# Optimization experiments

Measured on AMD Instinct MI355X. Metric: run time of the kernel, lower is better.

The kernel has to match this reference:

```python
import jax, jax.numpy as jnp
from jax import lax
import numpy as np

# LeNet-5 C3 sparse connectivity table (which S2 maps feed each C3 map)
IDX3 = np.array([[0,1,2],[1,2,3],[2,3,4],[3,4,5],[0,4,5],[0,1,5]])            # maps 0-5 (3 inputs)
IDX4 = np.array([[0,1,2,3],[1,2,3,4],[2,3,4,5],[0,3,4,5],[0,1,4,5],
                 [0,1,2,5],[0,1,3,4],[1,2,4,5],[0,2,3,5]])                    # maps 6-14 (4 inputs)


def _conv(x, w):
    return lax.conv_general_dilated(x, w, (1, 1), 'VALID',
                                    dimension_numbers=('NCHW', 'OIHW', 'NCHW'))


def _avgpool2(x):
    s = lax.reduce_window(x, 0.0, lax.add, (1, 1, 2, 2), (1, 1, 2, 2), 'VALID')
    return s * 0.25


def setup_inputs() -> dict:
    key = jax.random.key(0)
    ks = jax.random.split(key, 12)
    f = lambda k, shp: (jax.random.normal(k, shp, dtype=jnp.float32) * 0.1)
    return {
        'x':     jax.random.normal(ks[0], (8192, 1, 32, 32), dtype=jnp.float32),
        'c1_w':  f(ks[1], (6, 1, 5, 5)),   'c1_b': f(ks[2], (6,)),
        'c3_w3': f(ks[3], (6, 3, 5, 5)),   'c3_b3': f(ks[4], (6,)),
        'c3_w4': f(ks[5], (9, 4, 5, 5)),   'c3_b4': f(ks[6], (9,)),
        'c3_w6': f(ks[7], (1, 6, 5, 5)),   'c3_b6': f(ks[8], (1,)),
        'c5_w':  f(ks[9], (120, 16, 5, 5)), 'c5_b': f(ks[10], (120,)),
        'l1_w':  f(ks[11], (84, 120)), 'l1_b': jnp.zeros((84,), jnp.float32),
        'l2_w':  f(jax.random.fold_in(key, 99), (10, 84)), 'l2_b': jnp.zeros((10,), jnp.float32),
    }


def reference(x, c1_w, c1_b, c3_w3, c3_b3, c3_w4, c3_b4, c3_w6, c3_b6,
              c5_w, c5_b, l1_w, l1_b, l2_w, l2_b):
    # C1 + tanh + S2: [B,1,32,32] -> [B,6,14,14]
    out = jnp.tanh(_conv(x, c1_w) + c1_b[None, :, None, None])
    out = _avgpool2(out)

    # C3: fuse the 16 sparse-connectivity convs into one [16,6,5,5] conv
    # by scattering the small per-map kernels into a zero-padded weight.
    W = jnp.zeros((16, 6, 5, 5), dtype=out.dtype)
    W = W.at[np.arange(6)[:, None], IDX3].set(c3_w3)
    W = W.at[np.arange(6, 15)[:, None], IDX4].set(c3_w4)
    W = W.at[15].set(c3_w6[0])
    b = jnp.concatenate([c3_b3, c3_b4, c3_b6])
    out = _conv(out, W) + b[None, :, None, None]          # [B,16,10,10]

    out = _avgpool2(jnp.tanh(out))                        # [B,16,5,5]
    out = _conv(out, c5_w) + c5_b[None, :, None, None]    # [B,120,1,1]
    out = jnp.tanh(out[:, :, 0, 0])                       # [B,120]
    out = jnp.tanh(out @ l1_w.T + l1_b)                   # [B,84]
    return out @ l2_w.T + l2_b                            # [B,10]
```

## Files before the change

### kernel.cpp

```cpp
#include <hip/hip_runtime.h>

typedef float f32x4 __attribute__((ext_vector_type(4)));
typedef _Float16 h16;
typedef h16 half8 __attribute__((ext_vector_type(8)));

__device__ __forceinline__ float fast_tanh(float x) {
    float e = __expf(2.0f * x);
    return fmaf(-2.0f, __builtin_amdgcn_rcpf(e + 1.0f), 1.0f);
}
__device__ __forceinline__ half8 cvt8(float4 u0, float4 u1) {
    return (half8){(h16)u0.x,(h16)u0.y,(h16)u0.z,(h16)u0.w,
                   (h16)u1.x,(h16)u1.y,(h16)u1.z,(h16)u1.w};
}

#define S2IMGH 1576

#define C1_IMG 8

__global__ __launch_bounds__(256) void k_c1(
    const float* __restrict__ x, const float* __restrict__ c1_w,
    const float* __restrict__ c1_b, h16* __restrict__ s2g, int B)
{
    __shared__ __align__(16) h16 s2l[C1_IMG * S2IMGH];
    __shared__ float c1w_s[152];
    __shared__ float c1b_s[8];

    const int tid  = threadIdx.x;
    const int img0 = blockIdx.x * C1_IMG;
    const int nimg = min(C1_IMG, B - img0);
    if (nimg <= 0) return;

    if (tid < 150) c1w_s[tid] = c1_w[tid];
    if (tid < 6)   c1b_s[tid] = c1_b[tid];
    {
        const half8 z = {(h16)0,(h16)0,(h16)0,(h16)0,(h16)0,(h16)0,(h16)0,(h16)0};
        half8* zp = (half8*)s2l;
        for (int i = tid; i < C1_IMG * 197; i += 256) zp[i] = z;
    }
    __syncthreads();

    const int lane = tid & 63, wv = tid >> 6;
    const int nloc = lane & 15, q4 = lane >> 4;

    half8 bf[3][5];
    float bias[3];
    #pragma unroll
    for (int t = 0; t < 3; ++t) {
        const int tile = 3 * wv + t;
        const int map  = tile >> 1;
        const int j    = ((tile & 1) << 4) + nloc;
        bias[t] = c1b_s[map];
        #pragma unroll
        for (int ks = 0; ks < 5; ++ks) {
            half8 f;
            #pragma unroll
            for (int jj = 0; jj < 8; ++jj) {
                const int d = q4 * 8 + jj - j;
                f[jj] = (d >= 0 && d < 5) ? (h16)c1w_s[map * 25 + ks * 5 + d] : (h16)0;
            }
            bf[t][ks] = f;
        }
    }

    const int imgL = nloc >> 1, hf = nloc & 1;
    const int imgC = min(imgL, nimg - 1);
    const float* xg = x + (size_t)(img0 + imgC) * 1024 + hf * (14 * 32) + q4 * 8;
    half8 rf[5];
    #pragma unroll
    for (int r = 0; r < 5; ++r)
        rf[r] = cvt8(*(const float4*)(xg + r * 32), *(const float4*)(xg + r * 32 + 4));

    float t0[3][4];
    for (int cr = 0; cr < 14; ++cr) {
        f32x4 acc[3];
        #pragma unroll
        for (int t = 0; t < 3; ++t) acc[t] = (f32x4){0.f, 0.f, 0.f, 0.f};
        #pragma unroll
        for (int ks = 0; ks < 5; ++ks) {
            #pragma unroll
            for (int t = 0; t < 3; ++t)
                acc[t] = __builtin_amdgcn_mfma_f32_16x16x32_f16(rf[ks], bf[t][ks], acc[t], 0, 0, 0);
        }
        if ((cr & 1) == 0) {
            #pragma unroll
            for (int t = 0; t < 3; ++t)
                #pragma unroll
                for (int r = 0; r < 4; ++r)
                    t0[t][r] = fast_tanh(acc[t][r] + bias[t]);
        } else {
            #pragma unroll
            for (int t = 0; t < 3; ++t) {
                const int tile = 3 * wv + t;
                const int jp   = (((tile & 1) << 4) + nloc) >> 1;
                const int map  = tile >> 1;
                #pragma unroll
                for (int r = 0; r < 4; ++r) {
                    float s = t0[t][r] + fast_tanh(acc[t][r] + bias[t]);
                    float o = 0.25f * (s + __shfl_xor(s, 1));
                    const int m = q4 * 4 + r;
                    const int img = m >> 1, mh = m & 1;
                    const int ip  = (cr >> 1) + 7 * mh;
                    if (!(lane & 1) && jp < 14)
                        s2l[img * S2IMGH + (ip * 14 + jp) * 8 + map] = (h16)o;
                }
            }
        }
        if (cr < 13) {
            rf[0] = rf[1]; rf[1] = rf[2]; rf[2] = rf[3]; rf[3] = rf[4];
            rf[4] = cvt8(*(const float4*)(xg + (cr + 5) * 32),
                         *(const float4*)(xg + (cr + 5) * 32 + 4));
        }
    }
    __syncthreads();

    for (int i = tid; i < C1_IMG * 197; i += 256) {
        const int img = i / 197, c = i % 197;
        if (img < nimg)
            *(half8*)(s2g + (size_t)(img0 + img) * S2IMGH + c * 8) =
                *(const half8*)(s2l + img * S2IMGH + c * 8);
    }
}

__device__ __constant__ int C3_INV[16][6] = {
    {0,1,2,-1,-1,-1},{-1,0,1,2,-1,-1},{-1,-1,0,1,2,-1},{-1,-1,-1,0,1,2},
    {0,-1,-1,-1,1,2},{0,1,-1,-1,-1,2},
    {0,1,2,3,-1,-1},{-1,0,1,2,3,-1},{-1,-1,0,1,2,3},{0,-1,-1,1,2,3},
    {0,1,-1,-1,2,3},{0,1,2,-1,-1,3},{0,1,-1,2,3,-1},{-1,0,1,-1,2,3},
    {0,-1,1,2,-1,3},
    {0,1,2,3,4,5}
};

__global__ __launch_bounds__(256) void k_c3(
    const h16* __restrict__ s2g,
    const float* __restrict__ c3_w3, const float* __restrict__ c3_b3,
    const float* __restrict__ c3_w4, const float* __restrict__ c3_b4,
    const float* __restrict__ c3_w6, const float* __restrict__ c3_b6,
    h16* __restrict__ s4g, int B)
{
    __shared__ __align__(16) h16 s2i[16 * S2IMGH];

    const int tid  = threadIdx.x;
    const int img0 = blockIdx.x * 16;
    const int nimg = min(16, B - img0);
    if (nimg <= 0) return;

    {
        const half8 z = {(h16)0,(h16)0,(h16)0,(h16)0,(h16)0,(h16)0,(h16)0,(h16)0};
        const int img = tid >> 4;
        for (int c = (tid & 15); c < 197; c += 16)
            *(half8*)(s2i + img * S2IMGH + c * 8) =
                (img < nimg) ? *(const half8*)(s2g + (size_t)(img0 + img) * S2IMGH + c * 8)
                             : z;
    }

    const int lane = tid & 63, wv = tid >> 6;
    const int nloc = lane & 15, q4 = lane >> 4;

    half8 bf[7];
    #pragma unroll
    for (int t = 0; t < 7; ++t) {
        half8 f;
        int dr, dc; bool valid = true;
        if (t <= 4)      { dr = q4; dc = t; }
        else if (t == 5) { dr = 4; dc = q4; }
        else             { dr = 4; dc = 4; valid = (q4 == 0); }
        #pragma unroll
        for (int j = 0; j < 8; ++j) {
            float val = 0.0f;
            if (valid && j < 6) {
                const int cc = C3_INV[nloc][j];
                if (cc >= 0) {
                    const int off = dr * 5 + dc;
                    if (nloc < 6)       val = c3_w3[(nloc * 3 + cc) * 25 + off];
                    else if (nloc < 15) val = c3_w4[((nloc - 6) * 4 + cc) * 25 + off];
                    else                val = c3_w6[cc * 25 + off];
                }
            }
            f[j] = (h16)val;
        }
        bf[t] = f;
    }
    const float bias = (nloc < 6) ? c3_b3[nloc]
                     : (nloc < 15) ? c3_b4[nloc - 6] : c3_b6[0];
    __syncthreads();

    {
        const int abase = nloc * S2IMGH;
        for (int q = wv; q < 25; q += 4) {
            const int pr = q / 5, pc = q % 5;
            f32x4 acc[2][2];
            #pragma unroll
            for (int a = 0; a < 2; ++a)
                #pragma unroll
                for (int b2 = 0; b2 < 2; ++b2)
                    acc[a][b2] = (f32x4){0.f, 0.f, 0.f, 0.f};
            #pragma unroll
            for (int a = 0; a < 2; ++a) {
                #pragma unroll
                for (int b2 = 0; b2 < 2; ++b2) {
                    const int r = 2 * pr + a, col = 2 * pc + b2;
                    #pragma unroll
                    for (int t = 0; t < 5; ++t) {
                        half8 A = *(const half8*)(s2i + abase + ((r + q4) * 14 + col + t) * 8);
                        acc[a][b2] = __builtin_amdgcn_mfma_f32_16x16x32_f16(A, bf[t], acc[a][b2], 0, 0, 0);
                    }
                    half8 A5 = *(const half8*)(s2i + abase + ((r + 4) * 14 + col + q4) * 8);
                    acc[a][b2] = __builtin_amdgcn_mfma_f32_16x16x32_f16(A5, bf[5], acc[a][b2], 0, 0, 0);
                    half8 A6 = *(const half8*)(s2i + abase + ((r + 4) * 14 + col + 4) * 8);
                    acc[a][b2] = __builtin_amdgcn_mfma_f32_16x16x32_f16(A6, bf[6], acc[a][b2], 0, 0, 0);
                }
            }
            const int pos = pr * 5 + pc;
            #pragma unroll
            for (int rr = 0; rr < 4; ++rr) {
                const int img = q4 * 4 + rr;
                if (img < nimg) {
                    float s = fast_tanh(acc[0][0][rr] + bias) + fast_tanh(acc[0][1][rr] + bias)
                            + fast_tanh(acc[1][0][rr] + bias) + fast_tanh(acc[1][1][rr] + bias);
                    s4g[(size_t)(img0 + img) * 400 + nloc * 25 + pos] = (h16)(0.25f * s);
                }
            }
        }
    }
}

#define KT_IMG   16
#define S4L_STR  424
#define C5O_STR  136
#define F6L_STR  104
#define KT_S4L   0
#define KT_C5OL  (KT_IMG * S4L_STR * 2)
#define KT_F6L   (KT_C5OL + KT_IMG * C5O_STR * 2)
#define KT_BIAS  (KT_F6L + KT_IMG * F6L_STR * 2)
#define KT_SMEM  (KT_BIAS + 240 * 4)

__global__ __launch_bounds__(256) void k_tail(
    const h16* __restrict__ s4g,
    const float* __restrict__ c5_w, const float* __restrict__ c5_b,
    const float* __restrict__ l1_w, const float* __restrict__ l1_b,
    const float* __restrict__ l2_w, const float* __restrict__ l2_b,
    float* __restrict__ out, int B)
{
    __shared__ __align__(16) char smem[KT_SMEM];
    h16*   s4l   = (h16*)(smem + KT_S4L);
    h16*   c5ol  = (h16*)(smem + KT_C5OL);
    h16*   f6l   = (h16*)(smem + KT_F6L);
    float* c5b_s = (float*)(smem + KT_BIAS);
    float* l1b_s = c5b_s + 128;
    float* l2b_s = l1b_s + 96;

    const int tid  = threadIdx.x;
    const int img0 = blockIdx.x * KT_IMG;
    const int nimg = min(KT_IMG, B - img0);
    if (nimg <= 0) return;

    if (tid < 128)      c5b_s[tid] = (tid < 120) ? c5_b[tid] : 0.f;
    else if (tid < 224) { int i = tid - 128; l1b_s[i] = (i < 84) ? l1_b[i] : 0.f; }
    else if (tid < 240) { int i = tid - 224; l2b_s[i] = (i < 10) ? l2_b[i] : 0.f; }

    {
        const half8 z = {(h16)0,(h16)0,(h16)0,(h16)0,(h16)0,(h16)0,(h16)0,(h16)0};
        for (int i = tid; i < KT_IMG * 53; i += 256) {
            int img = i / 53, cc = i % 53;
            half8 v = z;
            if (img < nimg && cc < 50)
                v = *(const half8*)(s4g + (size_t)(img0 + img) * 400 + cc * 8);
            *(half8*)(s4l + img * S4L_STR + cc * 8) = v;
        }
    }
    __syncthreads();

    const int lane = tid & 63, wv = tid >> 6;
    const int nloc = lane & 15, q4 = lane >> 4;
    const half8 z8 = {(h16)0,(h16)0,(h16)0,(h16)0,(h16)0,(h16)0,(h16)0,(h16)0};

    {
        const int nb = wv * 2;
        f32x4 acc[2];
        acc[0] = (f32x4){0.f,0.f,0.f,0.f};
        acc[1] = (f32x4){0.f,0.f,0.f,0.f};
        for (int ks = 0; ks < 13; ++ks) {
            const int ka = ks * 32 + q4 * 8;
            half8 A = *(const half8*)(s4l + nloc * S4L_STR + ka);
            #pragma unroll
            for (int t = 0; t < 2; ++t) {
                const int n = (nb + t) * 16 + nloc;
                half8 Bf = z8;
                if (n < 120 && ka < 400) {
                    float4 u0 = *(const float4*)(c5_w + n * 400 + ka);
                    float4 u1 = *(const float4*)(c5_w + n * 400 + ka + 4);
                    Bf = cvt8(u0, u1);
                }
                acc[t] = __builtin_amdgcn_mfma_f32_16x16x32_f16(A, Bf, acc[t], 0, 0, 0);
            }
        }
        #pragma unroll
        for (int t = 0; t < 2; ++t) {
            const int o = (nb + t) * 16 + nloc;
            const float bo = c5b_s[o];
            #pragma unroll
            for (int r = 0; r < 4; ++r) {
                const int img = q4 * 4 + r;
                c5ol[img * C5O_STR + o] = (h16)fast_tanh(acc[t][r] + bo);
            }
        }
    }
    __syncthreads();

    if (wv < 3) {
        const int nb = wv * 2;
        f32x4 acc[2];
        acc[0] = (f32x4){0.f,0.f,0.f,0.f};
        acc[1] = (f32x4){0.f,0.f,0.f,0.f};
        for (int ks = 0; ks < 4; ++ks) {
            const int ka = ks * 32 + q4 * 8;
            half8 A = *(const half8*)(c5ol + nloc * C5O_STR + ka);
            #pragma unroll
            for (int t = 0; t < 2; ++t) {
                const int n = (nb + t) * 16 + nloc;
                half8 Bf = z8;
                if (n < 84 && ka < 120) {
                    float4 u0 = *(const float4*)(l1_w + n * 120 + ka);
                    float4 u1 = *(const float4*)(l1_w + n * 120 + ka + 4);
                    Bf = cvt8(u0, u1);
                }
                acc[t] = __builtin_amdgcn_mfma_f32_16x16x32_f16(A, Bf, acc[t], 0, 0, 0);
            }
        }
        #pragma unroll
        for (int t = 0; t < 2; ++t) {
            const int o = (nb + t) * 16 + nloc;
            const float bo = l1b_s[o];
            #pragma unroll
            for (int r = 0; r < 4; ++r) {
                const int img = q4 * 4 + r;
                f6l[img * F6L_STR + o] = (h16)fast_tanh(acc[t][r] + bo);
            }
        }
    }
    __syncthreads();

    if (wv == 0) {
        f32x4 acc = (f32x4){0.f,0.f,0.f,0.f};
        #pragma unroll
        for (int ks = 0; ks < 3; ++ks) {
            const int ka = ks * 32 + q4 * 8;
            half8 A = *(const half8*)(f6l + nloc * F6L_STR + ka);
            half8 Bf = z8;
            #pragma unroll
            for (int i = 0; i < 8; ++i) {
                const int k = ka + i;
                if (nloc < 10 && k < 84) Bf[i] = (h16)l2_w[nloc * 84 + k];
            }
            acc = __builtin_amdgcn_mfma_f32_16x16x32_f16(A, Bf, acc, 0, 0, 0);
        }
        if (nloc < 10) {
            #pragma unroll
            for (int r = 0; r < 4; ++r) {
                const int img = q4 * 4 + r;
                if (img < nimg)
                    out[(size_t)(img0 + img) * 10 + nloc] = acc[r] + l2b_s[nloc];
            }
        }
    }
}

extern "C" void kernel_launch(void* const* d_in, const int* in_sizes, int n_in,
                              void* d_out, int out_size, void* d_ws, size_t ws_size,
                              hipStream_t stream) {
    const float* x     = (const float*)d_in[0];
    const float* c1_w  = (const float*)d_in[1];
    const float* c1_b  = (const float*)d_in[2];
    const float* c3_w3 = (const float*)d_in[3];
    const float* c3_b3 = (const float*)d_in[4];
    const float* c3_w4 = (const float*)d_in[5];
    const float* c3_b4 = (const float*)d_in[6];
    const float* c3_w6 = (const float*)d_in[7];
    const float* c3_b6 = (const float*)d_in[8];
    const float* c5_w  = (const float*)d_in[9];
    const float* c5_b  = (const float*)d_in[10];
    const float* l1_w  = (const float*)d_in[11];
    const float* l1_b  = (const float*)d_in[12];
    const float* l2_w  = (const float*)d_in[13];
    const float* l2_b  = (const float*)d_in[14];
    float* out = (float*)d_out;

    const int B = in_sizes[0] / 1024;

    h16* s2g = (h16*)d_ws;
    h16* s4g = (h16*)((char*)d_ws + (size_t)B * S2IMGH * 2);

    k_c1<<<(B + C1_IMG - 1) / C1_IMG, 256, 0, stream>>>(x, c1_w, c1_b, s2g, B);
    k_c3<<<(B + 15) / 16, 256, 0, stream>>>(s2g, c3_w3, c3_b3, c3_w4, c3_b4,
                                            c3_w6, c3_b6, s4g, B);
    k_tail<<<(B + KT_IMG - 1) / KT_IMG, 256, 0, stream>>>(s4g, c5_w, c5_b,
                                                          l1_w, l1_b, l2_w, l2_b, out, B);
}
```

Measured before the change: 191.2 us.

## Split C1 and C3 blocks into two spatial halves to double grid size

```diff
diff --git a/kernel.cpp b/kernel.cpp
--- a/kernel.cpp
+++ b/kernel.cpp
@@ -17,69 +17,29 @@
 
 #define C1_IMG 8
 
-__global__ __launch_bounds__(256) void k_c1(
-    const float* __restrict__ x, const float* __restrict__ c1_w,
-    const float* __restrict__ c1_b, h16* __restrict__ s2g, int B)
+template<int BASE, int NITER>
+__device__ __forceinline__ void c1_phase(
+    const float* __restrict__ xg, const half8 (&bf)[3][5], const float (&bias)[3],
+    h16* __restrict__ s2l, int lane, int wv, int nloc, int q4)
 {
-    __shared__ __align__(16) h16 s2l[C1_IMG * S2IMGH];
-    __shared__ float c1w_s[152];
-    __shared__ float c1b_s[8];
-
-    const int tid  = threadIdx.x;
-    const int img0 = blockIdx.x * C1_IMG;
-    const int nimg = min(C1_IMG, B - img0);
-    if (nimg <= 0) return;
-
-    if (tid < 150) c1w_s[tid] = c1_w[tid];
-    if (tid < 6)   c1b_s[tid] = c1_b[tid];
-    {
-        const half8 z = {(h16)0,(h16)0,(h16)0,(h16)0,(h16)0,(h16)0,(h16)0,(h16)0};
-        half8* zp = (half8*)s2l;
-        for (int i = tid; i < C1_IMG * 197; i += 256) zp[i] = z;
-    }
-    __syncthreads();
-
-    const int lane = tid & 63, wv = tid >> 6;
-    const int nloc = lane & 15, q4 = lane >> 4;
-
-    half8 bf[3][5];
-    float bias[3];
+    half8 rw[NITER + 4];
     #pragma unroll
-    for (int t = 0; t < 3; ++t) {
-        const int tile = 3 * wv + t;
-        const int map  = tile >> 1;
-        const int j    = ((tile & 1) << 4) + nloc;
-        bias[t] = c1b_s[map];
+    for (int r = 0; r < NITER + 4; ++r)
+        rw[r] = cvt8(*(const float4*)(xg + (BASE + r) * 32),
+                     *(const float4*)(xg + (BASE + r) * 32 + 4));
+
+    float t0[3][4];
+    #pragma unroll
+    for (int cc = 0; cc < NITER; ++cc) {
+        const int cr = BASE + cc;
+        f32x4 acc[3];
+        #pragma unroll
+        for (int t = 0; t < 3; ++t) acc[t] = (f32x4){0.f, 0.f, 0.f, 0.f};
         #pragma unroll
         for (int ks = 0; ks < 5; ++ks) {
-            half8 f;
-            #pragma unroll
-            for (int jj = 0; jj < 8; ++jj) {
-                const int d = q4 * 8 + jj - j;
-                f[jj] = (d >= 0 && d < 5) ? (h16)c1w_s[map * 25 + ks * 5 + d] : (h16)0;
-            }
-            bf[t][ks] = f;
-        }
-    }
-
-    const int imgL = nloc >> 1, hf = nloc & 1;
-    const int imgC = min(imgL, nimg - 1);
-    const float* xg = x + (size_t)(img0 + imgC) * 1024 + hf * (14 * 32) + q4 * 8;
-    half8 rf[5];
-    #pragma unroll
-    for (int r = 0; r < 5; ++r)
-        rf[r] = cvt8(*(const float4*)(xg + r * 32), *(const float4*)(xg + r * 32 + 4));
-
-    float t0[3][4];
-    for (int cr = 0; cr < 14; ++cr) {
-        f32x4 acc[3];
-        #pragma unroll
-        for (int t = 0; t < 3; ++t) acc[t] = (f32x4){0.f, 0.f, 0.f, 0.f};
-        #pragma unroll
-        for (int ks = 0; ks < 5; ++ks) {
             #pragma unroll
             for (int t = 0; t < 3; ++t)
-                acc[t] = __builtin_amdgcn_mfma_f32_16x16x32_f16(rf[ks], bf[t][ks], acc[t], 0, 0, 0);
+                acc[t] = __builtin_amdgcn_mfma_f32_16x16x32_f16(rw[cc + ks], bf[t][ks], acc[t], 0, 0, 0);
         }
         if ((cr & 1) == 0) {
             #pragma unroll
@@ -105,19 +65,71 @@
                 }
             }
         }
-        if (cr < 13) {
-            rf[0] = rf[1]; rf[1] = rf[2]; rf[2] = rf[3]; rf[3] = rf[4];
-            rf[4] = cvt8(*(const float4*)(xg + (cr + 5) * 32),
-                         *(const float4*)(xg + (cr + 5) * 32 + 4));
-        }
-    }
-    __syncthreads();
-
-    for (int i = tid; i < C1_IMG * 197; i += 256) {
-        const int img = i / 197, c = i % 197;
+    }
+}
+
+__global__ __launch_bounds__(256) void k_c1(
+    const float* __restrict__ x, const float* __restrict__ c1_w,
+    const float* __restrict__ c1_b, h16* __restrict__ s2g, int B)
+{
+    __shared__ __align__(16) h16 s2l[C1_IMG * S2IMGH];
+    __shared__ float c1w_s[152];
+    __shared__ float c1b_s[8];
+
+    const int tid  = threadIdx.x;
+    const int ph   = blockIdx.x & 1;
+    const int img0 = (blockIdx.x >> 1) * C1_IMG;
+    const int nimg = min(C1_IMG, B - img0);
+    if (nimg <= 0) return;
+
+    if (tid < 150) c1w_s[tid] = c1_w[tid];
+    if (tid < 6)   c1b_s[tid] = c1_b[tid];
+    {
+        const half8 z = {(h16)0,(h16)0,(h16)0,(h16)0,(h16)0,(h16)0,(h16)0,(h16)0};
+        half8* zp = (half8*)s2l;
+        for (int i = tid; i < C1_IMG * 197; i += 256) zp[i] = z;
+    }
+    __syncthreads();
+
+    const int lane = tid & 63, wv = tid >> 6;
+    const int nloc = lane & 15, q4 = lane >> 4;
+
+    half8 bf[3][5];
+    float bias[3];
+    #pragma unroll
+    for (int t = 0; t < 3; ++t) {
+        const int tile = 3 * wv + t;
+        const int map  = tile >> 1;
+        const int j    = ((tile & 1) << 4) + nloc;
+        bias[t] = c1b_s[map];
+        #pragma unroll
+        for (int ks = 0; ks < 5; ++ks) {
+            half8 f;
+            #pragma unroll
+            for (int jj = 0; jj < 8; ++jj) {
+                const int d = q4 * 8 + jj - j;
+                f[jj] = (d >= 0 && d < 5) ? (h16)c1w_s[map * 25 + ks * 5 + d] : (h16)0;
+            }
+            bf[t][ks] = f;
+        }
+    }
+
+    const int imgL = nloc >> 1, hf = nloc & 1;
+    const int imgC = min(imgL, nimg - 1);
+    const float* xg = x + (size_t)(img0 + imgC) * 1024 + hf * (14 * 32) + q4 * 8;
+
+    if (ph == 0) c1_phase<0, 8>(xg, bf, bias, s2l, lane, wv, nloc, q4);
+    else         c1_phase<8, 6>(xg, bf, bias, s2l, lane, wv, nloc, q4);
+    __syncthreads();
+
+    const int nch = ph ? 84 : 112;
+    for (int i = tid; i < C1_IMG * nch; i += 256) {
+        const int img = i / nch, ii = i % nch;
+        const int pos = ph ? (ii < 42 ? 56 + ii : 112 + ii)
+                           : (ii < 56 ? ii : 42 + ii);
         if (img < nimg)
-            *(half8*)(s2g + (size_t)(img0 + img) * S2IMGH + c * 8) =
-                *(const half8*)(s2l + img * S2IMGH + c * 8);
+            *(half8*)(s2g + (size_t)(img0 + img) * S2IMGH + pos * 8) =
+                *(const half8*)(s2l + img * S2IMGH + pos * 8);
     }
 }
 
@@ -140,7 +152,8 @@
     __shared__ __align__(16) h16 s2i[16 * S2IMGH];
 
     const int tid  = threadIdx.x;
-    const int img0 = blockIdx.x * 16;
+    const int qs   = blockIdx.x & 1;
+    const int img0 = (blockIdx.x >> 1) * 16;
     const int nimg = min(16, B - img0);
     if (nimg <= 0) return;
 
@@ -186,7 +199,8 @@
 
     {
         const int abase = nloc * S2IMGH;
-        for (int q = wv; q < 25; q += 4) {
+        const int qlo = qs * 13, qhi = qs ? 25 : 13;
+        for (int q = qlo + wv; q < qhi; q += 4) {
             const int pr = q / 5, pc = q % 5;
             f32x4 acc[2][2];
             #pragma unroll
@@ -390,9 +404,9 @@
     h16* s2g = (h16*)d_ws;
     h16* s4g = (h16*)((char*)d_ws + (size_t)B * S2IMGH * 2);
 
-    k_c1<<<(B + C1_IMG - 1) / C1_IMG, 256, 0, stream>>>(x, c1_w, c1_b, s2g, B);
-    k_c3<<<(B + 15) / 16, 256, 0, stream>>>(s2g, c3_w3, c3_b3, c3_w4, c3_b4,
-                                            c3_w6, c3_b6, s4g, B);
+    k_c1<<<2 * ((B + C1_IMG - 1) / C1_IMG), 256, 0, stream>>>(x, c1_w, c1_b, s2g, B);
+    k_c3<<<2 * ((B + 15) / 16), 256, 0, stream>>>(s2g, c3_w3, c3_b3, c3_w4, c3_b4,
+                                                  c3_w6, c3_b6, s4g, B);
     k_tail<<<(B + KT_IMG - 1) / KT_IMG, 256, 0, stream>>>(s4g, c5_w, c5_b,
                                                           l1_w, l1_b, l2_w, l2_b, out, B);
 }
```

Measured after the change: 214.4 us. 12.1% more time.

## Fuse C3 and tail kernels, stage C1 input through LDS

Applied to the files above, without the earlier changes.

```diff
diff --git a/kernel.cpp b/kernel.cpp
--- a/kernel.cpp
+++ b/kernel.cpp
@@ -3,6 +3,7 @@
 typedef float f32x4 __attribute__((ext_vector_type(4)));
 typedef _Float16 h16;
 typedef h16 half8 __attribute__((ext_vector_type(8)));
+typedef h16 half4 __attribute__((ext_vector_type(4)));
 
 __device__ __forceinline__ float fast_tanh(float x) {
     float e = __expf(2.0f * x);
@@ -16,12 +17,14 @@
 #define S2IMGH 1576
 
 #define C1_IMG 8
+#define XROW  40
+#define XIMGH (32 * XROW + 8)
 
 __global__ __launch_bounds__(256) void k_c1(
     const float* __restrict__ x, const float* __restrict__ c1_w,
     const float* __restrict__ c1_b, h16* __restrict__ s2g, int B)
 {
-    __shared__ __align__(16) h16 s2l[C1_IMG * S2IMGH];
+    __shared__ __align__(16) h16 xs[C1_IMG * XIMGH];
     __shared__ float c1w_s[152];
     __shared__ float c1b_s[8];
 
@@ -32,10 +35,17 @@
 
     if (tid < 150) c1w_s[tid] = c1_w[tid];
     if (tid < 6)   c1b_s[tid] = c1_b[tid];
-    {
-        const half8 z = {(h16)0,(h16)0,(h16)0,(h16)0,(h16)0,(h16)0,(h16)0,(h16)0};
-        half8* zp = (half8*)s2l;
-        for (int i = tid; i < C1_IMG * 197; i += 256) zp[i] = z;
+
+    {
+        const float4* xg = (const float4*)(x + (size_t)img0 * 1024);
+        const int n4 = nimg * 256;
+        for (int i = tid; i < n4; i += 256) {
+            float4 v = xg[i];
+            int img = i >> 8, q = i & 255;
+            int row = q >> 3, col4 = (q & 7) << 2;
+            *(half4*)(xs + img * XIMGH + row * XROW + col4) =
+                (half4){(h16)v.x, (h16)v.y, (h16)v.z, (h16)v.w};
+        }
     }
     __syncthreads();
 
@@ -63,12 +73,10 @@
     }
 
     const int imgL = nloc >> 1, hf = nloc & 1;
-    const int imgC = min(imgL, nimg - 1);
-    const float* xg = x + (size_t)(img0 + imgC) * 1024 + hf * (14 * 32) + q4 * 8;
+    const h16* xrow = xs + imgL * XIMGH + hf * (14 * XROW) + q4 * 8;
     half8 rf[5];
     #pragma unroll
-    for (int r = 0; r < 5; ++r)
-        rf[r] = cvt8(*(const float4*)(xg + r * 32), *(const float4*)(xg + r * 32 + 4));
+    for (int r = 0; r < 5; ++r) rf[r] = *(const half8*)(xrow + r * XROW);
 
     float t0[3][4];
     for (int cr = 0; cr < 14; ++cr) {
@@ -100,26 +108,24 @@
                     const int m = q4 * 4 + r;
                     const int img = m >> 1, mh = m & 1;
                     const int ip  = (cr >> 1) + 7 * mh;
-                    if (!(lane & 1) && jp < 14)
-                        s2l[img * S2IMGH + (ip * 14 + jp) * 8 + map] = (h16)o;
+                    if (!(lane & 1) && jp < 14 && img < nimg)
+                        s2g[(size_t)(img0 + img) * S2IMGH + (ip * 14 + jp) * 8 + map] = (h16)o;
                 }
             }
         }
         if (cr < 13) {
             rf[0] = rf[1]; rf[1] = rf[2]; rf[2] = rf[3]; rf[3] = rf[4];
-            rf[4] = cvt8(*(const float4*)(xg + (cr + 5) * 32),
-                         *(const float4*)(xg + (cr + 5) * 32 + 4));
-        }
-    }
-    __syncthreads();
-
-    for (int i = tid; i < C1_IMG * 197; i += 256) {
-        const int img = i / 197, c = i % 197;
-        if (img < nimg)
-            *(half8*)(s2g + (size_t)(img0 + img) * S2IMGH + c * 8) =
-                *(const half8*)(s2l + img * S2IMGH + c * 8);
-    }
-}
+            rf[4] = *(const half8*)(xrow + (cr + 5) * XROW);
+        }
+    }
+}
+
+#define S4L_STR  424
+#define C5O_STR  136
+#define F6L_STR  104
+#define AL_C5O   (16 * S4L_STR)
+#define AL_F6    (AL_C5O + 16 * C5O_STR)
+#define ALIAS_H  (AL_F6 + 16 * F6L_STR)
 
 __device__ __constant__ int C3_INV[16][6] = {
     {0,1,2,-1,-1,-1},{-1,0,1,2,-1,-1},{-1,-1,0,1,2,-1},{-1,-1,-1,0,1,2},
@@ -130,19 +136,32 @@
     {0,1,2,3,4,5}
 };
 
-__global__ __launch_bounds__(256) void k_c3(
+__global__ __launch_bounds__(256) void k_c3t(
     const h16* __restrict__ s2g,
     const float* __restrict__ c3_w3, const float* __restrict__ c3_b3,
     const float* __restrict__ c3_w4, const float* __restrict__ c3_b4,
     const float* __restrict__ c3_w6, const float* __restrict__ c3_b6,
-    h16* __restrict__ s4g, int B)
+    const float* __restrict__ c5_w, const float* __restrict__ c5_b,
+    const float* __restrict__ l1_w, const float* __restrict__ l1_b,
+    const float* __restrict__ l2_w, const float* __restrict__ l2_b,
+    float* __restrict__ out, int B)
 {
     __shared__ __align__(16) h16 s2i[16 * S2IMGH];
+    __shared__ float c5b_s[128];
+    __shared__ float l1b_s[96];
+    __shared__ float l2b_s[16];
+    h16* s4l  = s2i;
+    h16* c5ol = s2i + AL_C5O;
+    h16* f6l  = s2i + AL_F6;
 
     const int tid  = threadIdx.x;
     const int img0 = blockIdx.x * 16;
     const int nimg = min(16, B - img0);
     if (nimg <= 0) return;
+
+    if (tid < 128)      c5b_s[tid] = (tid < 120) ? c5_b[tid] : 0.f;
+    else if (tid < 224) { int i = tid - 128; l1b_s[i] = (i < 84) ? l1_b[i] : 0.f; }
+    else if (tid < 240) { int i = tid - 224; l2b_s[i] = (i < 10) ? l2_b[i] : 0.f; }
 
     {
         const half8 z = {(h16)0,(h16)0,(h16)0,(h16)0,(h16)0,(h16)0,(h16)0,(h16)0};
@@ -155,6 +174,7 @@
 
     const int lane = tid & 63, wv = tid >> 6;
     const int nloc = lane & 15, q4 = lane >> 4;
+    const half8 z8 = {(h16)0,(h16)0,(h16)0,(h16)0,(h16)0,(h16)0,(h16)0,(h16)0};
 
     half8 bf[7];
     #pragma unroll
@@ -180,13 +200,15 @@
         }
         bf[t] = f;
     }
-    const float bias = (nloc < 6) ? c3_b3[nloc]
-                     : (nloc < 15) ? c3_b4[nloc - 6] : c3_b6[0];
-    __syncthreads();
-
+    const float c3bias = (nloc < 6) ? c3_b3[nloc]
+                       : (nloc < 15) ? c3_b4[nloc - 6] : c3_b6[0];
+    __syncthreads();
+
+    float res[7][4];
+    int nq = 0;
     {
         const int abase = nloc * S2IMGH;
-        for (int q = wv; q < 25; q += 4) {
+        for (int q = wv; q < 25; q += 4, ++nq) {
             const int pr = q / 5, pc = q % 5;
             f32x4 acc[2][2];
             #pragma unroll
@@ -210,69 +232,33 @@
                     acc[a][b2] = __builtin_amdgcn_mfma_f32_16x16x32_f16(A6, bf[6], acc[a][b2], 0, 0, 0);
                 }
             }
-            const int pos = pr * 5 + pc;
+            #pragma unroll
+            for (int rr = 0; rr < 4; ++rr) {
+                float s = fast_tanh(acc[0][0][rr] + c3bias) + fast_tanh(acc[0][1][rr] + c3bias)
+                        + fast_tanh(acc[1][0][rr] + c3bias) + fast_tanh(acc[1][1][rr] + c3bias);
+                res[nq][rr] = 0.25f * s;
+            }
+        }
+    }
+    __syncthreads();
+
+    {
+        half8* zp = (half8*)s4l;
+        for (int i = tid; i < (16 * S4L_STR) / 8; i += 256) zp[i] = z8;
+    }
+    __syncthreads();
+
+    {
+        int iq = 0;
+        for (int q = wv; q < 25; q += 4, ++iq) {
             #pragma unroll
             for (int rr = 0; rr < 4; ++rr) {
                 const int img = q4 * 4 + rr;
-                if (img < nimg) {
-                    float s = fast_tanh(acc[0][0][rr] + bias) + fast_tanh(acc[0][1][rr] + bias)
-                            + fast_tanh(acc[1][0][rr] + bias) + fast_tanh(acc[1][1][rr] + bias);
-                    s4g[(size_t)(img0 + img) * 400 + nloc * 25 + pos] = (h16)(0.25f * s);
-                }
-            }
-        }
-    }
-}
-
-#define KT_IMG   16
-#define S4L_STR  424
-#define C5O_STR  136
-#define F6L_STR  104
-#define KT_S4L   0
-#define KT_C5OL  (KT_IMG * S4L_STR * 2)
-#define KT_F6L   (KT_C5OL + KT_IMG * C5O_STR * 2)
-#define KT_BIAS  (KT_F6L + KT_IMG * F6L_STR * 2)
-#define KT_SMEM  (KT_BIAS + 240 * 4)
-
-__global__ __launch_bounds__(256) void k_tail(
-    const h16* __restrict__ s4g,
-    const float* __restrict__ c5_w, const float* __restrict__ c5_b,
-    const float* __restrict__ l1_w, const float* __restrict__ l1_b,
-    const float* __restrict__ l2_w, const float* __restrict__ l2_b,
-    float* __restrict__ out, int B)
-{
-    __shared__ __align__(16) char smem[KT_SMEM];
-    h16*   s4l   = (h16*)(smem + KT_S4L);
-    h16*   c5ol  = (h16*)(smem + KT_C5OL);
-    h16*   f6l   = (h16*)(smem + KT_F6L);
-    float* c5b_s = (float*)(smem + KT_BIAS);
-    float* l1b_s = c5b_s + 128;
-    float* l2b_s = l1b_s + 96;
-
-    const int tid  = threadIdx.x;
-    const int img0 = blockIdx.x * KT_IMG;
-    const int nimg = min(KT_IMG, B - img0);
-    if (nimg <= 0) return;
-
-    if (tid < 128)      c5b_s[tid] = (tid < 120) ? c5_b[tid] : 0.f;
-    else if (tid < 224) { int i = tid - 128; l1b_s[i] = (i < 84) ? l1_b[i] : 0.f; }
-    else if (tid < 240) { int i = tid - 224; l2b_s[i] = (i < 10) ? l2_b[i] : 0.f; }
-
-    {
-        const half8 z = {(h16)0,(h16)0,(h16)0,(h16)0,(h16)0,(h16)0,(h16)0,(h16)0};
-        for (int i = tid; i < KT_IMG * 53; i += 256) {
-            int img = i / 53, cc = i % 53;
-            half8 v = z;
-            if (img < nimg && cc < 50)
-                v = *(const half8*)(s4g + (size_t)(img0 + img) * 400 + cc * 8);
-            *(half8*)(s4l + img * S4L_STR + cc * 8) = v;
-        }
-    }
-    __syncthreads();
-
-    const int lane = tid & 63, wv = tid >> 6;
-    const int nloc = lane & 15, q4 = lane >> 4;
-    const half8 z8 = {(h16)0,(h16)0,(h16)0,(h16)0,(h16)0,(h16)0,(h16)0,(h16)0};
+                s4l[img * S4L_STR + nloc * 25 + q] = (h16)res[iq][rr];
+            }
+        }
+    }
+    __syncthreads();
 
     {
         const int nb = wv * 2;
@@ -388,11 +374,9 @@
     const int B = in_sizes[0] / 1024;
 
     h16* s2g = (h16*)d_ws;
-    h16* s4g = (h16*)((char*)d_ws + (size_t)B * S2IMGH * 2);
 
     k_c1<<<(B + C1_IMG - 1) / C1_IMG, 256, 0, stream>>>(x, c1_w, c1_b, s2g, B);
-    k_c3<<<(B + 15) / 16, 256, 0, stream>>>(s2g, c3_w3, c3_b3, c3_w4, c3_b4,
-                                            c3_w6, c3_b6, s4g, B);
-    k_tail<<<(B + KT_IMG - 1) / KT_IMG, 256, 0, stream>>>(s4g, c5_w, c5_b,
-                                                          l1_w, l1_b, l2_w, l2_b, out, B);
-}
+    k_c3t<<<(B + 15) / 16, 256, 0, stream>>>(s2g, c3_w3, c3_b3, c3_w4, c3_b4,
+                                             c3_w6, c3_b6, c5_w, c5_b,
+                                             l1_w, l1_b, l2_w, l2_b, out, B);
+}
```

After: 174.9 us. 1.09x faster.
